# Optimization experiments

Measured on AMD Instinct MI355X. Metric: run time of the kernel, lower is better.

Reference implementation:

```python
import jax, jax.numpy as jnp
import numpy as np

B, T, C = 4, 2048, 1024
E, D, TOP_K = 8, 3072, 2


def setup_inputs() -> dict:
    key = jax.random.key(0)
    ks = jax.random.split(key, 6)
    s_c = 1.0 / np.sqrt(C)
    s_d = 1.0 / np.sqrt(D)
    return {
        "x": jax.random.normal(ks[0], (B, T, C), dtype=jnp.float32),
        "router_w": jax.random.uniform(ks[1], (E, C), jnp.float32, -s_c, s_c),
        "W1": jax.random.uniform(ks[2], (E, C, D), jnp.float32, -s_c, s_c),
        "b1": jax.random.uniform(ks[3], (E, D), jnp.float32, -s_c, s_c),
        "W2": jax.random.uniform(ks[4], (E, D, C), jnp.float32, -s_d, s_d),
        "b2": jax.random.uniform(ks[5], (E, C), jnp.float32, -s_d, s_d),
    }


def reference(x, router_w, W1, b1, W2, b2):
    b, t, c = x.shape
    xf = x.reshape(b * t, c)                      # [N, C]
    n = xf.shape[0]
    logits = xf @ router_w.T                       # [N, E]
    probs = jax.nn.softmax(logits, axis=-1)
    topw, topi = jax.lax.top_k(probs, TOP_K)       # [N, k]
    topw = topw / jnp.sum(topw, axis=-1, keepdims=True)
    # scatter normalized top-k weights into [N, E] combine weights
    mask = jnp.zeros_like(probs).at[jnp.arange(n)[:, None], topi].set(topw)
    # dense expert MLPs (zero combine weight == token not routed to expert)
    h = jax.nn.gelu(jnp.einsum('nc,ecd->ned', xf, W1) + b1, approximate=False)
    y = jnp.einsum('ned,edc->nec', h, W2) + b2     # [N, E, C]
    out = jnp.einsum('ne,nec->nc', mask, y).reshape(b, t, c)
    aux_loss = jnp.zeros((), dtype=x.dtype)        # eval mode
    return out, aux_loss
```

## Files before the change

kernel.cpp:

```cpp
#include <hip/hip_runtime.h>
#include <math.h>

#define N_TOK 8192
#define C_DIM 1024
#define D_DIM 3072
#define E_NUM 8
#define SEG 128
#define MAXB 136

typedef unsigned short u16;
typedef unsigned int u32;
typedef __attribute__((ext_vector_type(8))) short bf16x8;
typedef __attribute__((ext_vector_type(4))) float f32x4;

__device__ __forceinline__ u16 f2bf(float f) {
  u32 u = __builtin_bit_cast(unsigned int, f);
  u = (u + 0x7FFFu + ((u >> 16) & 1u)) >> 16;
  return (u16)u;
}

__device__ __forceinline__ void gl_lds16(const void* g, void* l) {
  __builtin_amdgcn_global_load_lds(
      (const __attribute__((address_space(1))) unsigned int*)g,
      (__attribute__((address_space(3))) unsigned int*)l, 16, 0, 0);
}

template<int N> __device__ __forceinline__ void wait_bar() {
  if constexpr (N == 0) asm volatile("s_waitcnt vmcnt(0)\n\ts_barrier" ::: "memory");
  else if constexpr (N == 4) asm volatile("s_waitcnt vmcnt(4)\n\ts_barrier" ::: "memory");
}
__device__ __forceinline__ void bar_only() {
  asm volatile("s_barrier" ::: "memory");
}

__global__ void zero_init_kernel(float* __restrict__ out, int n, int* __restrict__ cnt) {
  int i = blockIdx.x * 256 + threadIdx.x;
  if (i < n) out[i] = 0.0f;
  if (i < E_NUM) cnt[i] = 0;
}

__global__ void transpose_w1_kernel(const float* __restrict__ W1, u16* __restrict__ W1t) {
  __shared__ float t[32][33];
  const int e = blockIdx.z;
  const int d0 = blockIdx.x * 32, c0 = blockIdx.y * 32;
  const int tx = threadIdx.x, ty = threadIdx.y;
#pragma unroll
  for (int i = 0; i < 4; i++)
    t[ty + i * 8][tx] = W1[((size_t)e * C_DIM + c0 + ty + i * 8) * D_DIM + d0 + tx];
  __syncthreads();
#pragma unroll
  for (int i = 0; i < 4; i++)
    W1t[((size_t)e * D_DIM + d0 + ty + i * 8) * C_DIM + c0 + tx] = f2bf(t[tx][ty + i * 8]);
}

__global__ void transpose_w2_kernel(const float* __restrict__ W2, u16* __restrict__ W2t) {
  __shared__ float t[32][33];
  const int e = blockIdx.z;
  const int c0 = blockIdx.x * 32, d0 = blockIdx.y * 32;
  const int tx = threadIdx.x, ty = threadIdx.y;
#pragma unroll
  for (int i = 0; i < 4; i++)
    t[ty + i * 8][tx] = W2[((size_t)e * D_DIM + d0 + ty + i * 8) * C_DIM + c0 + tx];
  __syncthreads();
#pragma unroll
  for (int i = 0; i < 4; i++)
    W2t[((size_t)e * C_DIM + c0 + ty + i * 8) * D_DIM + d0 + tx] = f2bf(t[tx][ty + i * 8]);
}

__global__ void router_kernel(const float* __restrict__ x, const float* __restrict__ rw,
                              int* __restrict__ cnt, int* __restrict__ list,
                              float* __restrict__ wl) {
  const int lane = threadIdx.x & 63;
  const int n = blockIdx.x * 4 + (threadIdx.x >> 6);
  const float* xr = x + (size_t)n * C_DIM;
  double acc[E_NUM];
#pragma unroll
  for (int e = 0; e < E_NUM; e++) acc[e] = 0.0;
  for (int c = lane; c < C_DIM; c += 64) {
    float xv = xr[c];
#pragma unroll
    for (int e = 0; e < E_NUM; e++) acc[e] += (double)xv * (double)rw[e * C_DIM + c];
  }
#pragma unroll
  for (int e = 0; e < E_NUM; e++) {
    double v = acc[e];
#pragma unroll
    for (int off = 32; off > 0; off >>= 1) v += __shfl_down(v, off, 64);
    acc[e] = v;
  }
  if (lane == 0) {
    int i0 = 0;
#pragma unroll
    for (int e = 1; e < E_NUM; e++) if (acc[e] > acc[i0]) i0 = e;
    int i1 = (i0 == 0) ? 1 : 0;
#pragma unroll
    for (int e = 0; e < E_NUM; e++) if (e != i0 && acc[e] > acc[i1]) i1 = e;
    double d = acc[i0] - acc[i1];
    double w0 = 1.0 / (1.0 + exp(-d));
    double w1 = 1.0 - w0;
    int p0 = atomicAdd(&cnt[i0], 1);
    list[i0 * N_TOK + p0] = n; wl[i0 * N_TOK + p0] = (float)w0;
    int p1 = atomicAdd(&cnt[i1], 1);
    list[i1 * N_TOK + p1] = n; wl[i1 * N_TOK + p1] = (float)w1;
  }
}

__global__ void prefix_kernel(const int* __restrict__ cnt, int* __restrict__ rowbase,
                              int* __restrict__ btab) {
  if (threadIdx.x == 0) {
    int s = 0, nb = 0;
    for (int e = 0; e < E_NUM; e++) {
      rowbase[e] = s;
      for (int m0 = 0; m0 < cnt[e]; m0 += SEG) { btab[2 * nb] = e; btab[2 * nb + 1] = m0; nb++; }
      s += cnt[e];
    }
    for (; nb < MAXB; nb++) { btab[2 * nb] = -1; btab[2 * nb + 1] = 0; }
  }
}

__global__ void gather_x_kernel(const float* __restrict__ x, const int* __restrict__ cnt,
                                const int* __restrict__ rowbase, const int* __restrict__ list,
                                u16* __restrict__ Xg) {
  const int e = blockIdx.y;
  const int p = blockIdx.x * 4 + (threadIdx.x >> 6);
  if (p >= cnt[e]) return;
  const int lane = threadIdx.x & 63;
  const int tok = list[e * N_TOK + p];
  const float* src = x + (size_t)tok * C_DIM;
  u16* dst = Xg + (size_t)(rowbase[e] + p) * C_DIM;
#pragma unroll
  for (int i = 0; i < 4; i++) {
    float4 v = *(const float4*)(src + lane * 4 + i * 256);
    ushort4 o;
    o.x = f2bf(v.x); o.y = f2bf(v.y); o.z = f2bf(v.z); o.w = f2bf(v.w);
    *(ushort4*)(dst + lane * 4 + i * 256) = o;
  }
}

template<int NN0, int K, int EPI>
__global__ __launch_bounds__(256, 4) void gemm_tlp_kernel(
    const u16* __restrict__ A, const u16* __restrict__ Wt, const float* __restrict__ bias_,
    const int* __restrict__ btab, const int* __restrict__ cnt, const int* __restrict__ rowbase,
    const int* __restrict__ list, const float* __restrict__ wl,
    u16* __restrict__ hout, float* __restrict__ out) {
  constexpr int NTOT = NN0 * 128;
  constexpr int NT = K / 32;
  constexpr int TOT = MAXB * NN0;

  __shared__ __align__(16) u16 ldsA[2 * 128 * 32];
  __shared__ __align__(16) u16 ldsB[2 * 128 * 32];

  const int L = (blockIdx.x & 7) * (TOT / 8) + (blockIdx.x >> 3);
  const int bx = L / NN0;
  const int n0 = (L % NN0) * 128;

  const int e = btab[bx * 2];
  if (e < 0) return;
  const int m0 = btab[bx * 2 + 1];
  const int count = cnt[e];
  const int rb = rowbase[e];

  const int tid = threadIdx.x;
  const int lane = tid & 63;
  const int wid = tid >> 6;
  const int wm = (wid >> 1) * 64;
  const int wn = (wid & 1) * 64;
  const int l15 = lane & 15, l4 = lane >> 4;

  const int arow0 = tid >> 2, pos = (tid & 3) * 8;
  const u16* aptr0 = A + (size_t)(rb + min(m0 + arow0, count - 1)) * K + pos;
  const u16* aptr1 = A + (size_t)(rb + min(m0 + arow0 + 64, count - 1)) * K + pos;
  const u16* bptr0 = Wt + ((size_t)e * NTOT + n0 + arow0) * K + pos;
  const u16* bptr1 = Wt + ((size_t)e * NTOT + n0 + arow0 + 64) * K + pos;

  const int paoff = (wm + l15) * 32 + l4 * 8;
  const int pboff = (wn + l15) * 32 + l4 * 8;

  f32x4 acc[4][4];
#pragma unroll
  for (int i = 0; i < 4; i++)
#pragma unroll
    for (int j = 0; j < 4; j++) acc[i][j] = {0.f, 0.f, 0.f, 0.f};

  auto STAGE = [&](int t, int b) {
    u16* da = ldsA + b * 4096 + tid * 8;
    u16* db = ldsB + b * 4096 + tid * 8;
    const int ko = t * 32;
    gl_lds16(aptr0 + ko, da);
    gl_lds16(aptr1 + ko, da + 2048);
    gl_lds16(bptr0 + ko, db);
    gl_lds16(bptr1 + ko, db + 2048);
  };

  auto PHASE = [&](int b) {
    const u16* pa = ldsA + b * 4096 + paoff;
    const u16* pb = ldsB + b * 4096 + pboff;
    bf16x8 av[4], bv[4];
#pragma unroll
    for (int i = 0; i < 4; i++) av[i] = *(const bf16x8*)(pa + i * 512);
#pragma unroll
    for (int j = 0; j < 4; j++) bv[j] = *(const bf16x8*)(pb + j * 512);
#pragma unroll
    for (int i = 0; i < 4; i++)
#pragma unroll
      for (int j = 0; j < 4; j++)
        acc[i][j] = __builtin_amdgcn_mfma_f32_16x16x32_bf16(av[i], bv[j], acc[i][j], 0, 0, 0);
  };

  STAGE(0, 0);
#pragma unroll 2
  for (int t = 0; t < NT - 1; ++t) {
    STAGE(t + 1, (t + 1) & 1);
    wait_bar<4>();
    PHASE(t & 1);
    bar_only();
  }
  wait_bar<0>();
  PHASE((NT - 1) & 1);

  if constexpr (EPI == 1) {
#pragma unroll
    for (int i = 0; i < 4; i++) {
      const int rloc = wm + i * 16 + l4 * 4;
#pragma unroll
      for (int j = 0; j < 4; j++) {
        const int col = n0 + wn + j * 16 + l15;
        const float bias = bias_[e * NTOT + col];
#pragma unroll
        for (int r = 0; r < 4; r++) {
          const int m = m0 + rloc + r;
          if (m < count) {
            float v = acc[i][j][r] + bias;
            float g = 0.5f * v * (1.0f + erff(v * 0.70710678118654752f));
            hout[(size_t)(rb + m) * D_DIM + col] = f2bf(g);
          }
        }
      }
    }
  } else {
    const int* lst = list + e * N_TOK;
    const float* wlst = wl + e * N_TOK;
#pragma unroll
    for (int i = 0; i < 4; i++) {
      const int rloc = wm + i * 16 + l4 * 4;
#pragma unroll
      for (int j = 0; j < 4; j++) {
        const int col = n0 + wn + j * 16 + l15;
        const float bias = bias_[e * NTOT + col];
#pragma unroll
        for (int r = 0; r < 4; r++) {
          const int m = m0 + rloc + r;
          if (m < count) {
            const int tk = lst[m];
            atomicAdd(out + (size_t)tk * C_DIM + col, wlst[m] * (acc[i][j][r] + bias));
          }
        }
      }
    }
  }
}

extern "C" void kernel_launch(void* const* d_in, const int* in_sizes, int n_in,
                              void* d_out, int out_size, void* d_ws, size_t ws_size,
                              hipStream_t stream) {
  const float* x  = (const float*)d_in[0];
  const float* rw = (const float*)d_in[1];
  const float* W1 = (const float*)d_in[2];
  const float* b1 = (const float*)d_in[3];
  const float* W2 = (const float*)d_in[4];
  const float* b2 = (const float*)d_in[5];
  float* out = (float*)d_out;

  char* ws = (char*)d_ws;
  u16* W1t    = (u16*)(ws);
  u16* Xg     = (u16*)(ws + 50331648);
  u16* W2t    = (u16*)(ws + 50331648);
  int* cnt    = (int*)(ws + 100663296);
  int* rowbase= (int*)(ws + 100663552);
  int* list   = (int*)(ws + 100663808);
  float* wl   = (float*)(ws + 100925952);
  int* btab   = (int*)(ws + 101188096);
  u16* h      = (u16*)(ws + 101190656);

  zero_init_kernel<<<(out_size + 255) / 256, 256, 0, stream>>>(out, out_size, cnt);
  router_kernel<<<N_TOK / 4, 256, 0, stream>>>(x, rw, cnt, list, wl);
  prefix_kernel<<<1, 64, 0, stream>>>(cnt, rowbase, btab);
  gather_x_kernel<<<dim3(N_TOK / 4, E_NUM), 256, 0, stream>>>(x, cnt, rowbase, list, Xg);
  transpose_w1_kernel<<<dim3(D_DIM / 32, C_DIM / 32, E_NUM), dim3(32, 8), 0, stream>>>(W1, W1t);
  gemm_tlp_kernel<24, C_DIM, 1><<<MAXB * 24, 256, 0, stream>>>(
      Xg, W1t, b1, btab, cnt, rowbase, list, wl, h, out);
  transpose_w2_kernel<<<dim3(C_DIM / 32, D_DIM / 32, E_NUM), dim3(32, 8), 0, stream>>>(W2, W2t);
  gemm_tlp_kernel<8, D_DIM, 2><<<MAXB * 8, 256, 0, stream>>>(
      h, W2t, b2, btab, cnt, rowbase, list, wl, h, out);
}
```

Baseline: 689.3 us.

## Vectorize weight transpose kernels and group GEMM tiles into 4x4 cohorts

Replaces the two 32x32 weight transpose/convert kernels with one templated 64x64 tile kernel. It reads float4 and writes eight bf16 values per 16-byte store, to cut memory instructions on the weight conversion pass. It also remaps the GEMM block index so that 16 consecutive blocks cover a 4x4 group of row-block by column-tile pairs, which should improve L2 reuse of A and W tiles. The remap assumes NN0 is divisible by 4 and MAXB by 4, which holds for 24, 8 and 136. The transpose now reads LDS column-strided with a 65 pad, which may cause some bank conflicts.

```diff
diff --git a/kernel.cpp b/kernel.cpp
--- a/kernel.cpp
+++ b/kernel.cpp
@@ -39,32 +39,33 @@
   if (i < E_NUM) cnt[i] = 0;
 }
 
-__global__ void transpose_w1_kernel(const float* __restrict__ W1, u16* __restrict__ W1t) {
-  __shared__ float t[32][33];
+template<int R, int CC>
+__global__ __launch_bounds__(256) void transpose_conv_kernel(
+    const float* __restrict__ in, u16* __restrict__ outp) {
+  __shared__ float t[64][65];
   const int e = blockIdx.z;
-  const int d0 = blockIdx.x * 32, c0 = blockIdx.y * 32;
-  const int tx = threadIdx.x, ty = threadIdx.y;
-#pragma unroll
-  for (int i = 0; i < 4; i++)
-    t[ty + i * 8][tx] = W1[((size_t)e * C_DIM + c0 + ty + i * 8) * D_DIM + d0 + tx];
+  const int r0 = blockIdx.y * 64;
+  const int c0 = blockIdx.x * 64;
+  const int tid = threadIdx.x;
+  const int lr = tid >> 4;
+  const int lc = (tid & 15) * 4;
+#pragma unroll
+  for (int i = 0; i < 4; i++) {
+    float4 v = *(const float4*)(in + ((size_t)e * R + r0 + lr + i * 16) * CC + c0 + lc);
+    t[lr + i * 16][lc] = v.x; t[lr + i * 16][lc + 1] = v.y;
+    t[lr + i * 16][lc + 2] = v.z; t[lr + i * 16][lc + 3] = v.w;
+  }
   __syncthreads();
-#pragma unroll
-  for (int i = 0; i < 4; i++)
-    W1t[((size_t)e * D_DIM + d0 + ty + i * 8) * C_DIM + c0 + tx] = f2bf(t[tx][ty + i * 8]);
-}
-
-__global__ void transpose_w2_kernel(const float* __restrict__ W2, u16* __restrict__ W2t) {
-  __shared__ float t[32][33];
-  const int e = blockIdx.z;
-  const int c0 = blockIdx.x * 32, d0 = blockIdx.y * 32;
-  const int tx = threadIdx.x, ty = threadIdx.y;
-#pragma unroll
-  for (int i = 0; i < 4; i++)
-    t[ty + i * 8][tx] = W2[((size_t)e * D_DIM + d0 + ty + i * 8) * C_DIM + c0 + tx];
-  __syncthreads();
-#pragma unroll
-  for (int i = 0; i < 4; i++)
-    W2t[((size_t)e * C_DIM + c0 + ty + i * 8) * D_DIM + d0 + tx] = f2bf(t[tx][ty + i * 8]);
+  const int orow = tid >> 3;
+  const int oc = (tid & 7) * 8;
+#pragma unroll
+  for (int i = 0; i < 2; i++) {
+    const int d = orow + i * 32;
+    union { u16 s[8]; uint4 v; } o;
+#pragma unroll
+    for (int j = 0; j < 8; j++) o.s[j] = f2bf(t[oc + j][d]);
+    *(uint4*)(outp + ((size_t)e * CC + c0 + d) * R + r0 + oc) = o.v;
+  }
 }
 
 __global__ void router_kernel(const float* __restrict__ x, const float* __restrict__ rw,
@@ -145,14 +146,18 @@
     u16* __restrict__ hout, float* __restrict__ out) {
   constexpr int NTOT = NN0 * 128;
   constexpr int NT = K / 32;
+  constexpr int NG = NN0 / 4;
   constexpr int TOT = MAXB * NN0;
 
   __shared__ __align__(16) u16 ldsA[2 * 128 * 32];
   __shared__ __align__(16) u16 ldsB[2 * 128 * 32];
 
   const int L = (blockIdx.x & 7) * (TOT / 8) + (blockIdx.x >> 3);
-  const int bx = L / NN0;
-  const int n0 = (L % NN0) * 128;
+  const int coh = L >> 4, r = L & 15;
+  const int bxg = coh / NG;
+  const int n0g = coh % NG;
+  const int bx = bxg * 4 + (r & 3);
+  const int n0 = (n0g * 4 + (r >> 2)) * 128;
 
   const int e = btab[bx * 2];
   if (e < 0) return;
@@ -227,10 +232,10 @@
         const int col = n0 + wn + j * 16 + l15;
         const float bias = bias_[e * NTOT + col];
 #pragma unroll
-        for (int r = 0; r < 4; r++) {
-          const int m = m0 + rloc + r;
+        for (int rr = 0; rr < 4; rr++) {
+          const int m = m0 + rloc + rr;
           if (m < count) {
-            float v = acc[i][j][r] + bias;
+            float v = acc[i][j][rr] + bias;
             float g = 0.5f * v * (1.0f + erff(v * 0.70710678118654752f));
             hout[(size_t)(rb + m) * D_DIM + col] = f2bf(g);
           }
@@ -248,11 +253,11 @@
         const int col = n0 + wn + j * 16 + l15;
         const float bias = bias_[e * NTOT + col];
 #pragma unroll
-        for (int r = 0; r < 4; r++) {
-          const int m = m0 + rloc + r;
+        for (int rr = 0; rr < 4; rr++) {
+          const int m = m0 + rloc + rr;
           if (m < count) {
             const int tk = lst[m];
-            atomicAdd(out + (size_t)tk * C_DIM + col, wlst[m] * (acc[i][j][r] + bias));
+            atomicAdd(out + (size_t)tk * C_DIM + col, wlst[m] * (acc[i][j][rr] + bias));
           }
         }
       }
@@ -286,10 +291,10 @@
   router_kernel<<<N_TOK / 4, 256, 0, stream>>>(x, rw, cnt, list, wl);
   prefix_kernel<<<1, 64, 0, stream>>>(cnt, rowbase, btab);
   gather_x_kernel<<<dim3(N_TOK / 4, E_NUM), 256, 0, stream>>>(x, cnt, rowbase, list, Xg);
-  transpose_w1_kernel<<<dim3(D_DIM / 32, C_DIM / 32, E_NUM), dim3(32, 8), 0, stream>>>(W1, W1t);
+  transpose_conv_kernel<C_DIM, D_DIM><<<dim3(D_DIM / 64, C_DIM / 64, E_NUM), 256, 0, stream>>>(W1, W1t);
   gemm_tlp_kernel<24, C_DIM, 1><<<MAXB * 24, 256, 0, stream>>>(
       Xg, W1t, b1, btab, cnt, rowbase, list, wl, h, out);
-  transpose_w2_kernel<<<dim3(C_DIM / 32, D_DIM / 32, E_NUM), dim3(32, 8), 0, stream>>>(W2, W2t);
+  transpose_conv_kernel<D_DIM, C_DIM><<<dim3(C_DIM / 64, D_DIM / 64, E_NUM), 256, 0, stream>>>(W2, W2t);
   gemm_tlp_kernel<8, D_DIM, 2><<<MAXB * 8, 256, 0, stream>>>(
       h, W2t, b2, btab, cnt, rowbase, list, wl, h, out);
 }
```

After: 671.5 us. 1.03x faster.
